# Kernel tuning notes

Hardware: AMD Instinct MI355X
Metric: run time of the kernel (lower is better)

## Reference

```python
import jax, jax.numpy as jnp
import numpy as np

EMBED_DIM = 1024
NUM_HEADS = 16
HEAD_DIM = EMBED_DIM // NUM_HEADS


def setup_inputs() -> dict:
    key = jax.random.key(0)
    ks = jax.random.split(key, 9)
    B, S, E, hd = 2, 2048, EMBED_DIM, HEAD_DIM
    s_e = 1.0 / np.sqrt(E)
    return {
        "x": jax.random.normal(ks[0], (B, S, E), dtype=jnp.float32),
        "wq": jax.random.uniform(ks[1], (E, E), jnp.float32, -s_e, s_e),
        "bq": jax.random.uniform(ks[2], (E,), jnp.float32, -s_e, s_e),
        "wk": jax.random.uniform(ks[3], (E, hd), jnp.float32, -s_e, s_e),
        "bk": jax.random.uniform(ks[4], (hd,), jnp.float32, -s_e, s_e),
        "wv": jax.random.uniform(ks[5], (E, hd), jnp.float32, -s_e, s_e),
        "bv": jax.random.uniform(ks[6], (hd,), jnp.float32, -s_e, s_e),
        "wo": jax.random.uniform(ks[7], (E, E), jnp.float32, -s_e, s_e),
        "bo": jax.random.uniform(ks[8], (E,), jnp.float32, -s_e, s_e),
    }


def reference(x, wq, bq, wk, bk, wv, bv, wo, bo):
    B, S, E = x.shape
    H, hd = NUM_HEADS, HEAD_DIM
    # projections
    q = (x @ wq + bq).reshape(B, S, H, hd)          # [B,S,H,hd]
    k = x @ wk + bk                                  # [B,S,hd] shared across heads
    v = x @ wv + bv                                  # [B,S,hd]
    scale = 1.0 / np.sqrt(hd).astype(np.float32)
    # scores: [B,H,S_q,S_k]
    scores = jnp.einsum('bqhd,bkd->bhqk', q, k) * scale
    attn = jax.nn.softmax(scores, axis=-1)
    out = jnp.einsum('bhqk,bkd->bqhd', attn, v).reshape(B, S, E)
    return out @ wo + bo
```

## Files before the change

kernel.cpp:

```cpp
#include <hip/hip_runtime.h>
#include <stdint.h>

#define SLEN 2048
#define EDIM 1024
#define NH 16
#define HD 64
#define QLD 1152

typedef unsigned short u16;
typedef short bf8 __attribute__((ext_vector_type(8)));
typedef float f4 __attribute__((ext_vector_type(4)));
typedef bf8 bf8_a __attribute__((may_alias));
typedef uint2 uint2_a __attribute__((may_alias));
typedef uint4 uint4_a __attribute__((may_alias));

__device__ __forceinline__ float bf2f(u16 u) {
  union { unsigned u; float f; } c; c.u = ((unsigned)u) << 16; return c.f;
}
__device__ __forceinline__ u16 f2bf(float x) {
  union { __bf16 h; u16 u; } c; c.h = (__bf16)x; return c.u;
}
__device__ __forceinline__ unsigned pk2bf(float a, float b) {
  union { __bf16 h[2]; unsigned u; } c;
  c.h[0] = (__bf16)a; c.h[1] = (__bf16)b;
  return c.u;
}
__device__ __forceinline__ void async_cp16(u16* lds, const u16* g) {
  __builtin_amdgcn_global_load_lds((__attribute__((address_space(1))) void*)g,
                                   (__attribute__((address_space(3))) void*)lds,
                                   16, 0, 0);
}

__global__ void probe_dtype(const unsigned* __restrict__ x, int* __restrict__ flag) {
  __shared__ int red[256];
  const int t = threadIdx.x;
  int cnt = 0;
  for (int i = t; i < 1024; i += 256) {
    unsigned e = (x[i] >> 7) & 0xFFu;
    cnt += (e >= 0x70u && e <= 0x8Fu) ? 1 : 0;
  }
  red[t] = cnt;
  __syncthreads();
  for (int s = 128; s > 0; s >>= 1) {
    if (t < s) red[t] += red[t + s];
    __syncthreads();
  }
  if (t == 0) *flag = (red[0] >= 512) ? 1 : 0;
}

__global__ void convert_x(const void* __restrict__ src, u16* __restrict__ dst,
                          const int* __restrict__ flag) {
  const int i = (blockIdx.x * 256 + threadIdx.x) * 8;
  if (*flag) {
    *(uint4_a*)&dst[i] = *(const uint4_a*)((const u16*)src + i);
  } else {
    const float* s = (const float*)src;
    u16 tmp[8];
#pragma unroll
    for (int j = 0; j < 8; ++j) tmp[j] = f2bf(s[i + j]);
    *(uint4_a*)&dst[i] = *(const uint4_a*)tmp;
  }
}

__device__ __forceinline__ void tcvt_tile(const void* src, int srcLd,
                                          u16* dst, int dstLd, int r0, int c0,
                                          bool isbf) {
  __shared__ u16 tile[64][65];
  const int t = threadIdx.x;
#pragma unroll
  for (int i = 0; i < 16; ++i) {
    int e = i * 256 + t, rr = e >> 6, cc = e & 63;
    size_t idx = (size_t)(r0 + rr) * srcLd + c0 + cc;
    tile[rr][cc] = isbf ? ((const u16*)src)[idx] : f2bf(((const float*)src)[idx]);
  }
  __syncthreads();
#pragma unroll
  for (int i = 0; i < 16; ++i) {
    int e = i * 256 + t, j = e >> 6, ii = e & 63;
    dst[(size_t)(c0 + j) * dstLd + r0 + ii] = tile[ii][j];
  }
}

__global__ void tcvt_qo(const void* wq, u16* wT, const void* wo, u16* woT,
                        const int* __restrict__ flag) {
  const bool isbf = (*flag != 0);
  const int yy = blockIdx.y;
  if (yy < 16) tcvt_tile(wq, 1024, wT, 1024, blockIdx.x * 64, yy * 64, isbf);
  else         tcvt_tile(wo, 1024, woT, 1024, blockIdx.x * 64, (yy - 16) * 64, isbf);
}
__global__ void tcvt_kv(const void* wk, const void* wv, u16* wT,
                        const int* __restrict__ flag) {
  const bool isbf = (*flag != 0);
  if (blockIdx.y == 0)
    tcvt_tile(wk, 64, wT + (size_t)1024 * 1024, 1024, blockIdx.x * 64, 0, isbf);
  else
    tcvt_tile(wv, 64, wT + (size_t)1088 * 1024, 1024, blockIdx.x * 64, 0, isbf);
}

__global__ void tpose_v(const u16* __restrict__ qkvb, u16* __restrict__ vTb) {
  __shared__ u16 tile[64][65];
  const int b = blockIdx.y, r0 = blockIdx.x * 64;
  const u16* src = qkvb + (size_t)b * SLEN * QLD + 1088;
  u16* dst = vTb + (size_t)b * 64 * SLEN;
  const int t = threadIdx.x;
#pragma unroll
  for (int i = 0; i < 16; ++i) {
    int e = i * 256 + t, rr = e >> 6, cc = e & 63;
    tile[rr][cc] = src[(size_t)(r0 + rr) * QLD + cc];
  }
  __syncthreads();
#pragma unroll
  for (int i = 0; i < 16; ++i) {
    int e = i * 256 + t, j = e >> 6, ii = e & 63;
    dst[(size_t)j * SLEN + r0 + ii] = tile[ii][j];
  }
}

__global__ void prep_bias(const void* bq, const void* bk, const void* bv,
                          const void* bo, float* biasQKV, float* biasOut,
                          const int* __restrict__ flag) {
  const bool isbf = (*flag != 0);
  int i = blockIdx.x * 256 + threadIdx.x;
  auto rd = [&](const void* p, int idx) -> float {
    return isbf ? bf2f(((const u16*)p)[idx]) : ((const float*)p)[idx];
  };
  if (i < 1024) biasQKV[i] = rd(bq, i);
  else if (i < 1088) biasQKV[i] = rd(bk, i - 1024);
  else if (i < 1152) biasQKV[i] = rd(bv, i - 1088);
  int j = i - 1152;
  if (j >= 0 && j < 1024) biasOut[j] = rd(bo, j);
}

__global__ __launch_bounds__(256) void gemm_bt_bias(
    const u16* __restrict__ A, const u16* __restrict__ Bt,
    const float* __restrict__ bias, void* __restrict__ C, int K, int ldc,
    int ofp32) {
  __shared__ __align__(16) u16 As[128 * 64];
  __shared__ __align__(16) u16 Bs[128 * 64];
  const int tn0 = blockIdx.x * 128, tm0 = blockIdx.y * 128;
  const int tid = threadIdx.x, wave = tid >> 6, lane = tid & 63;
  const int quad = lane >> 4, l16 = lane & 15;
  const int wm = wave & 1, wn = wave >> 1;

  f4 acc[4][4];
#pragma unroll
  for (int i = 0; i < 4; ++i)
#pragma unroll
    for (int j = 0; j < 4; ++j) acc[i][j] = f4{0.f, 0.f, 0.f, 0.f};

  int slot[4]; size_t aoff[4], boff[4];
#pragma unroll
  for (int i = 0; i < 4; ++i) {
    int s = i * 256 + tid, m = s >> 3, kc = s & 7, c = (kc - m) & 7;
    slot[i] = s;
    aoff[i] = (size_t)(tm0 + m) * K + c * 8;
    boff[i] = (size_t)(tn0 + m) * K + c * 8;
  }
  int ard[4][2], brd[4][2];
#pragma unroll
  for (int mi = 0; mi < 4; ++mi) {
    int m = wm * 64 + mi * 16 + l16;
#pragma unroll
    for (int kk = 0; kk < 2; ++kk)
      ard[mi][kk] = (m * 8 + (((kk * 4 + quad) + m) & 7)) * 8;
  }
#pragma unroll
  for (int ni = 0; ni < 4; ++ni) {
    int n = wn * 64 + ni * 16 + l16;
#pragma unroll
    for (int kk = 0; kk < 2; ++kk)
      brd[ni][kk] = (n * 8 + (((kk * 4 + quad) + n) & 7)) * 8;
  }

  const int kIt = K >> 6;
  for (int it = 0; it < kIt; ++it) {
    __syncthreads();
    const size_t kb = (size_t)it * 64;
#pragma unroll
    for (int i = 0; i < 4; ++i) {
      async_cp16(&As[slot[i] * 8], A + aoff[i] + kb);
      async_cp16(&Bs[slot[i] * 8], Bt + boff[i] + kb);
    }
    __syncthreads();
#pragma unroll
    for (int kk = 0; kk < 2; ++kk) {
      bf8 af[4], bfr[4];
#pragma unroll
      for (int mi = 0; mi < 4; ++mi) af[mi] = *(const bf8_a*)&As[ard[mi][kk]];
#pragma unroll
      for (int ni = 0; ni < 4; ++ni) bfr[ni] = *(const bf8_a*)&Bs[brd[ni][kk]];
#pragma unroll
      for (int mi = 0; mi < 4; ++mi)
#pragma unroll
        for (int ni = 0; ni < 4; ++ni)
          acc[mi][ni] = __builtin_amdgcn_mfma_f32_16x16x32_bf16(
              af[mi], bfr[ni], acc[mi][ni], 0, 0, 0);
    }
  }

  float bv[4];
#pragma unroll
  for (int ni = 0; ni < 4; ++ni) bv[ni] = bias[tn0 + wn * 64 + ni * 16 + l16];
#pragma unroll
  for (int mi = 0; mi < 4; ++mi) {
    int row0 = tm0 + wm * 64 + mi * 16 + quad * 4;
#pragma unroll
    for (int ni = 0; ni < 4; ++ni) {
      int col = tn0 + wn * 64 + ni * 16 + l16;
#pragma unroll
      for (int r = 0; r < 4; ++r) {
        float v = acc[mi][ni][r] + bv[ni];
        if (ofp32) ((float*)C)[(size_t)(row0 + r) * ldc + col] = v;
        else       ((u16*)C)[(size_t)(row0 + r) * ldc + col] = f2bf(v);
      }
    }
  }
}

__global__ __launch_bounds__(256, 2) void attn_kernel(
    const u16* __restrict__ qkv, const u16* __restrict__ vT,
    u16* __restrict__ aout) {
  __shared__ __align__(16) u16 Kf[8192];
  __shared__ __align__(16) u16 Vf[8192];
  __shared__ __align__(16) u16 Ps[16384];
  const int qt = blockIdx.x, bh = blockIdx.y, b = bh >> 4, h = bh & 15;
  const int tid = threadIdx.x, wave = tid >> 6, lane = tid & 63;
  const int quad = lane >> 4, l16 = lane & 15;

#pragma unroll
  for (int i = 0; i < 4; ++i) {
    int d = i * 256 + tid;
    int kk = d >> 9, g = (d >> 6) & 7, qd = (d >> 4) & 3, r16 = d & 15;
    async_cp16(&Kf[d * 8],
               qkv + (size_t)(b * SLEN + qt * 128 + g * 16 + r16) * QLD +
                   h * HD + (kk * 4 + qd) * 8);
  }
  __syncthreads();
  bf8 bq[2][2];
#pragma unroll
  for (int nt = 0; nt < 2; ++nt)
#pragma unroll
    for (int kk = 0; kk < 2; ++kk)
      bq[nt][kk] = *(const bf8_a*)&Kf[((kk * 8 + wave * 2 + nt) * 64 + lane) * 8];

  f4 acc_o[2][4];
#pragma unroll
  for (int i = 0; i < 2; ++i)
#pragma unroll
    for (int j = 0; j < 4; ++j) acc_o[i][j] = f4{0.f, 0.f, 0.f, 0.f};
  f4 lr4[2] = {f4{0.f, 0.f, 0.f, 0.f}, f4{0.f, 0.f, 0.f, 0.f}};
  const float C1 = 0.125f * 1.44269504089f;

  for (int kt = 0; kt < 16; ++kt) {
    __syncthreads();
#pragma unroll
    for (int i = 0; i < 4; ++i) {
      int d = i * 256 + tid;
      int kk = d >> 9, k8 = (d >> 6) & 7, qd = (d >> 4) & 3, r16 = d & 15;
      async_cp16(&Kf[d * 8],
                 qkv + (size_t)(b * SLEN + kt * 128 + k8 * 16 + r16) * QLD +
                     EDIM + (kk * 4 + qd) * 8);
    }
#pragma unroll
    for (int i = 0; i < 4; ++i) {
      int d = i * 256 + tid;
      int k4 = d >> 8, ni = (d >> 6) & 3, qd = (d >> 4) & 3, r16 = d & 15;
      async_cp16(&Vf[d * 8],
                 vT + (size_t)(b * 64 + ni * 16 + r16) * SLEN + kt * 128 +
                     (k4 * 4 + qd) * 8);
    }
    __syncthreads();

    f4 st[8][2];
#pragma unroll
    for (int k8 = 0; k8 < 8; ++k8)
#pragma unroll
      for (int nt = 0; nt < 2; ++nt) st[k8][nt] = f4{0.f, 0.f, 0.f, 0.f};
#pragma unroll
    for (int kk = 0; kk < 2; ++kk)
#pragma unroll
      for (int k8 = 0; k8 < 8; ++k8) {
        bf8 ak = *(const bf8_a*)&Kf[((kk * 8 + k8) * 64 + lane) * 8];
#pragma unroll
        for (int nt = 0; nt < 2; ++nt)
          st[k8][nt] = __builtin_amdgcn_mfma_f32_16x16x32_bf16(ak, bq[nt][kk], st[k8][nt], 0, 0, 0);
      }

#pragma unroll
    for (int nt = 0; nt < 2; ++nt)
#pragma unroll
      for (int k8 = 0; k8 < 8; ++k8) {
        f4 pe;
        pe[0] = __builtin_amdgcn_exp2f(st[k8][nt][0] * C1);
        pe[1] = __builtin_amdgcn_exp2f(st[k8][nt][1] * C1);
        pe[2] = __builtin_amdgcn_exp2f(st[k8][nt][2] * C1);
        pe[3] = __builtin_amdgcn_exp2f(st[k8][nt][3] * C1);
        lr4[nt] += pe;
        uint2 pk;
        pk.x = pk2bf(pe[0], pe[1]);
        pk.y = pk2bf(pe[2], pe[3]);
        int c = nt * 256 + (k8 >> 1) * 64 + (((k8 << 1) + (quad >> 1)) & 3) * 16 + l16;
        *(uint2_a*)&Ps[(wave * 512 + c) * 8 + (quad & 1) * 4] = pk;
      }
    __syncthreads();

#pragma unroll
    for (int k4 = 0; k4 < 4; ++k4) {
      bf8 ap[2];
#pragma unroll
      for (int mt = 0; mt < 2; ++mt)
        ap[mt] = *(const bf8_a*)&Ps[(wave * 512 + mt * 256 + k4 * 64 + quad * 16 + l16) * 8];
#pragma unroll
      for (int ni = 0; ni < 4; ++ni) {
        bf8 bv = *(const bf8_a*)&Vf[((k4 * 4 + ni) * 64 + lane) * 8];
#pragma unroll
        for (int mt = 0; mt < 2; ++mt)
          acc_o[mt][ni] = __builtin_amdgcn_mfma_f32_16x16x32_bf16(ap[mt], bv, acc_o[mt][ni], 0, 0, 0);
      }
    }
  }

  float ls[2];
#pragma unroll
  for (int nt = 0; nt < 2; ++nt) {
    float s = (lr4[nt][0] + lr4[nt][1]) + (lr4[nt][2] + lr4[nt][3]);
    s += __shfl_xor(s, 16, 64);
    s += __shfl_xor(s, 32, 64);
    ls[nt] = s;
  }
#pragma unroll
  for (int mt = 0; mt < 2; ++mt)
#pragma unroll
    for (int r = 0; r < 4; ++r) {
      float li = __shfl(ls[mt], quad * 4 + r, 64);
      float inv = 1.f / li;
      size_t row = (size_t)(b * SLEN + qt * 128 + wave * 32 + mt * 16 + quad * 4 + r);
#pragma unroll
      for (int ni = 0; ni < 4; ++ni)
        aout[row * EDIM + h * HD + ni * 16 + l16] = f2bf(acc_o[mt][ni][r] * inv);
    }
}

extern "C" void kernel_launch(void* const* d_in, const int* in_sizes, int n_in,
                              void* d_out, int out_size, void* d_ws, size_t ws_size,
                              hipStream_t stream) {
  const void* x  = d_in[0];
  const void* wq = d_in[1];
  const void* bq = d_in[2];
  const void* wk = d_in[3];
  const void* bk = d_in[4];
  const void* wv = d_in[5];
  const void* bv = d_in[6];
  const void* wo = d_in[7];
  const void* bo = d_in[8];

  char* ws = (char*)d_ws;
  size_t off = 0;
  auto carve = [&](size_t bytes) {
    void* p = ws + off;
    off = (off + bytes + 255) & ~(size_t)255;
    return p;
  };
  int* dflag   = (int*)carve(256);
  u16* xbf     = (u16*)carve((size_t)4096 * EDIM * 2);
  u16* wT      = (u16*)carve((size_t)1152 * 1024 * 2);
  u16* woT     = (u16*)carve((size_t)1024 * 1024 * 2);
  float* bQKV  = (float*)carve(1152 * 4);
  float* bOut  = (float*)carve(1024 * 4);
  u16* qkvb    = (u16*)carve((size_t)4096 * QLD * 2);
  u16* vTb     = (u16*)carve((size_t)2 * 64 * SLEN * 2);
  u16* aob     = (u16*)carve((size_t)4096 * EDIM * 2);

  probe_dtype<<<dim3(1), 256, 0, stream>>>((const unsigned*)x, dflag);
  convert_x<<<dim3(2048), 256, 0, stream>>>(x, xbf, dflag);
  tcvt_qo<<<dim3(16, 32), 256, 0, stream>>>(wq, wT, wo, woT, dflag);
  tcvt_kv<<<dim3(16, 2), 256, 0, stream>>>(wk, wv, wT, dflag);
  prep_bias<<<dim3(9), 256, 0, stream>>>(bq, bk, bv, bo, bQKV, bOut, dflag);

  gemm_bt_bias<<<dim3(9, 32), 256, 0, stream>>>(xbf, wT, bQKV, qkvb, 1024, QLD, 0);

  tpose_v<<<dim3(32, 2), 256, 0, stream>>>(qkvb, vTb);

  attn_kernel<<<dim3(16, 32), 256, 0, stream>>>(qkvb, vTb, aob);

  gemm_bt_bias<<<dim3(8, 32), 256, 0, stream>>>(aob, woT, bOut, d_out, 1024, 1024, 1);
}
```

Baseline: 210.5 us.

## Drop dtype probe, merge prep kernels, fuse V transpose, shrink GEMM tiles, per-chunk softmax

Removes the runtime dtype probe and assumes fp32 inputs, then merges the weight transpose and bias prep into one launch. The V transpose now happens in the QKV GEMM epilogue instead of a separate kernel. GEMM M-tiles shrink to 64 rows to launch more blocks. The attention kernel computes scores and P chunk by chunk per wave, which cuts P shared memory and raises the occupancy hint to 4 blocks per CU. Fewer launches and better occupancy come at the cost of less B-tile reuse in the GEMMs and of dropping bf16 input support.

```diff
diff --git a/kernel.cpp b/kernel.cpp
--- a/kernel.cpp
+++ b/kernel.cpp
@@ -14,9 +14,6 @@
 typedef uint2 uint2_a __attribute__((may_alias));
 typedef uint4 uint4_a __attribute__((may_alias));
 
-__device__ __forceinline__ float bf2f(u16 u) {
-  union { unsigned u; float f; } c; c.u = ((unsigned)u) << 16; return c.f;
-}
 __device__ __forceinline__ u16 f2bf(float x) {
   union { __bf16 h; u16 u; } c; c.h = (__bf16)x; return c.u;
 }
@@ -31,47 +28,22 @@
                                    16, 0, 0);
 }
 
-__global__ void probe_dtype(const unsigned* __restrict__ x, int* __restrict__ flag) {
-  __shared__ int red[256];
-  const int t = threadIdx.x;
-  int cnt = 0;
-  for (int i = t; i < 1024; i += 256) {
-    unsigned e = (x[i] >> 7) & 0xFFu;
-    cnt += (e >= 0x70u && e <= 0x8Fu) ? 1 : 0;
-  }
-  red[t] = cnt;
-  __syncthreads();
-  for (int s = 128; s > 0; s >>= 1) {
-    if (t < s) red[t] += red[t + s];
-    __syncthreads();
-  }
-  if (t == 0) *flag = (red[0] >= 512) ? 1 : 0;
-}
-
-__global__ void convert_x(const void* __restrict__ src, u16* __restrict__ dst,
-                          const int* __restrict__ flag) {
+__global__ void convert_x(const float* __restrict__ src, u16* __restrict__ dst) {
   const int i = (blockIdx.x * 256 + threadIdx.x) * 8;
-  if (*flag) {
-    *(uint4_a*)&dst[i] = *(const uint4_a*)((const u16*)src + i);
-  } else {
-    const float* s = (const float*)src;
-    u16 tmp[8];
-#pragma unroll
-    for (int j = 0; j < 8; ++j) tmp[j] = f2bf(s[i + j]);
-    *(uint4_a*)&dst[i] = *(const uint4_a*)tmp;
-  }
-}
-
-__device__ __forceinline__ void tcvt_tile(const void* src, int srcLd,
-                                          u16* dst, int dstLd, int r0, int c0,
-                                          bool isbf) {
+  u16 tmp[8];
+#pragma unroll
+  for (int j = 0; j < 8; ++j) tmp[j] = f2bf(src[i + j]);
+  *(uint4_a*)&dst[i] = *(const uint4_a*)tmp;
+}
+
+__device__ __forceinline__ void tcvt_tile(const float* src, int srcLd,
+                                          u16* dst, int dstLd, int r0, int c0) {
   __shared__ u16 tile[64][65];
   const int t = threadIdx.x;
 #pragma unroll
   for (int i = 0; i < 16; ++i) {
     int e = i * 256 + t, rr = e >> 6, cc = e & 63;
-    size_t idx = (size_t)(r0 + rr) * srcLd + c0 + cc;
-    tile[rr][cc] = isbf ? ((const u16*)src)[idx] : f2bf(((const float*)src)[idx]);
+    tile[rr][cc] = f2bf(src[(size_t)(r0 + rr) * srcLd + c0 + cc]);
   }
   __syncthreads();
 #pragma unroll
@@ -81,85 +53,57 @@
   }
 }
 
-__global__ void tcvt_qo(const void* wq, u16* wT, const void* wo, u16* woT,
-                        const int* __restrict__ flag) {
-  const bool isbf = (*flag != 0);
+__global__ void prep_w(const float* wq, const float* wk, const float* wv,
+                       const float* wo, const float* bq, const float* bk,
+                       const float* bv, const float* bo,
+                       u16* wT, u16* woT, float* bQKV, float* bOut) {
   const int yy = blockIdx.y;
-  if (yy < 16) tcvt_tile(wq, 1024, wT, 1024, blockIdx.x * 64, yy * 64, isbf);
-  else         tcvt_tile(wo, 1024, woT, 1024, blockIdx.x * 64, (yy - 16) * 64, isbf);
-}
-__global__ void tcvt_kv(const void* wk, const void* wv, u16* wT,
-                        const int* __restrict__ flag) {
-  const bool isbf = (*flag != 0);
-  if (blockIdx.y == 0)
-    tcvt_tile(wk, 64, wT + (size_t)1024 * 1024, 1024, blockIdx.x * 64, 0, isbf);
-  else
-    tcvt_tile(wv, 64, wT + (size_t)1088 * 1024, 1024, blockIdx.x * 64, 0, isbf);
-}
-
-__global__ void tpose_v(const u16* __restrict__ qkvb, u16* __restrict__ vTb) {
-  __shared__ u16 tile[64][65];
-  const int b = blockIdx.y, r0 = blockIdx.x * 64;
-  const u16* src = qkvb + (size_t)b * SLEN * QLD + 1088;
-  u16* dst = vTb + (size_t)b * 64 * SLEN;
-  const int t = threadIdx.x;
-#pragma unroll
-  for (int i = 0; i < 16; ++i) {
-    int e = i * 256 + t, rr = e >> 6, cc = e & 63;
-    tile[rr][cc] = src[(size_t)(r0 + rr) * QLD + cc];
-  }
-  __syncthreads();
-#pragma unroll
-  for (int i = 0; i < 16; ++i) {
-    int e = i * 256 + t, j = e >> 6, ii = e & 63;
-    dst[(size_t)j * SLEN + r0 + ii] = tile[ii][j];
-  }
-}
-
-__global__ void prep_bias(const void* bq, const void* bk, const void* bv,
-                          const void* bo, float* biasQKV, float* biasOut,
-                          const int* __restrict__ flag) {
-  const bool isbf = (*flag != 0);
-  int i = blockIdx.x * 256 + threadIdx.x;
-  auto rd = [&](const void* p, int idx) -> float {
-    return isbf ? bf2f(((const u16*)p)[idx]) : ((const float*)p)[idx];
-  };
-  if (i < 1024) biasQKV[i] = rd(bq, i);
-  else if (i < 1088) biasQKV[i] = rd(bk, i - 1024);
-  else if (i < 1152) biasQKV[i] = rd(bv, i - 1088);
-  int j = i - 1152;
-  if (j >= 0 && j < 1024) biasOut[j] = rd(bo, j);
+  if (yy < 16) tcvt_tile(wq, 1024, wT, 1024, blockIdx.x * 64, yy * 64);
+  else if (yy < 32) tcvt_tile(wo, 1024, woT, 1024, blockIdx.x * 64, (yy - 16) * 64);
+  else if (yy == 32) tcvt_tile(wk, 64, wT + (size_t)1024 * 1024, 1024, blockIdx.x * 64, 0);
+  else if (yy == 33) tcvt_tile(wv, 64, wT + (size_t)1088 * 1024, 1024, blockIdx.x * 64, 0);
+  else {
+    int i = blockIdx.x * 256 + threadIdx.x;
+    if (i < 1024) bQKV[i] = bq[i];
+    else if (i < 1088) bQKV[i] = bk[i - 1024];
+    else if (i < 1152) bQKV[i] = bv[i - 1088];
+    int j = i - 1152;
+    if (j >= 0 && j < 1024) bOut[j] = bo[j];
+  }
 }
 
 __global__ __launch_bounds__(256) void gemm_bt_bias(
     const u16* __restrict__ A, const u16* __restrict__ Bt,
     const float* __restrict__ bias, void* __restrict__ C, int K, int ldc,
-    int ofp32) {
-  __shared__ __align__(16) u16 As[128 * 64];
+    int ofp32, u16* __restrict__ vtb) {
+  __shared__ __align__(16) u16 As[64 * 64];
   __shared__ __align__(16) u16 Bs[128 * 64];
-  const int tn0 = blockIdx.x * 128, tm0 = blockIdx.y * 128;
+  const int tn0 = blockIdx.x * 128, tm0 = blockIdx.y * 64;
   const int tid = threadIdx.x, wave = tid >> 6, lane = tid & 63;
   const int quad = lane >> 4, l16 = lane & 15;
   const int wm = wave & 1, wn = wave >> 1;
 
-  f4 acc[4][4];
-#pragma unroll
-  for (int i = 0; i < 4; ++i)
+  f4 acc[2][4];
+#pragma unroll
+  for (int i = 0; i < 2; ++i)
 #pragma unroll
     for (int j = 0; j < 4; ++j) acc[i][j] = f4{0.f, 0.f, 0.f, 0.f};
 
-  int slot[4]; size_t aoff[4], boff[4];
+  int aslot[2], bslot[4]; size_t aoff[2], boff[4];
+#pragma unroll
+  for (int i = 0; i < 2; ++i) {
+    int s = i * 256 + tid, m = s >> 3, kc = s & 7, c = (kc - m) & 7;
+    aslot[i] = s; aoff[i] = (size_t)(tm0 + m) * K + c * 8;
+  }
 #pragma unroll
   for (int i = 0; i < 4; ++i) {
-    int s = i * 256 + tid, m = s >> 3, kc = s & 7, c = (kc - m) & 7;
-    slot[i] = s;
-    aoff[i] = (size_t)(tm0 + m) * K + c * 8;
-    boff[i] = (size_t)(tn0 + m) * K + c * 8;
-  }
-  int ard[4][2], brd[4][2];
-#pragma unroll
-  for (int mi = 0; mi < 4; ++mi) {
-    int m = wm * 64 + mi * 16 + l16;
+    int s = i * 256 + tid, n = s >> 3, kc = s & 7, c = (kc - n) & 7;
+    bslot[i] = s; boff[i] = (size_t)(tn0 + n) * K + c * 8;
+  }
+  int ard[2][2], brd[4][2];
+#pragma unroll
+  for (int mi = 0; mi < 2; ++mi) {
+    int m = wm * 32 + mi * 16 + l16;
 #pragma unroll
     for (int kk = 0; kk < 2; ++kk)
       ard[mi][kk] = (m * 8 + (((kk * 4 + quad) + m) & 7)) * 8;
@@ -177,20 +121,19 @@
     __syncthreads();
     const size_t kb = (size_t)it * 64;
 #pragma unroll
-    for (int i = 0; i < 4; ++i) {
-      async_cp16(&As[slot[i] * 8], A + aoff[i] + kb);
-      async_cp16(&Bs[slot[i] * 8], Bt + boff[i] + kb);
-    }
+    for (int i = 0; i < 2; ++i) async_cp16(&As[aslot[i] * 8], A + aoff[i] + kb);
+#pragma unroll
+    for (int i = 0; i < 4; ++i) async_cp16(&Bs[bslot[i] * 8], Bt + boff[i] + kb);
     __syncthreads();
 #pragma unroll
     for (int kk = 0; kk < 2; ++kk) {
-      bf8 af[4], bfr[4];
-#pragma unroll
-      for (int mi = 0; mi < 4; ++mi) af[mi] = *(const bf8_a*)&As[ard[mi][kk]];
+      bf8 af[2], bfr[4];
+#pragma unroll
+      for (int mi = 0; mi < 2; ++mi) af[mi] = *(const bf8_a*)&As[ard[mi][kk]];
 #pragma unroll
       for (int ni = 0; ni < 4; ++ni) bfr[ni] = *(const bf8_a*)&Bs[brd[ni][kk]];
 #pragma unroll
-      for (int mi = 0; mi < 4; ++mi)
+      for (int mi = 0; mi < 2; ++mi)
 #pragma unroll
         for (int ni = 0; ni < 4; ++ni)
           acc[mi][ni] = __builtin_amdgcn_mfma_f32_16x16x32_bf16(
@@ -202,27 +145,40 @@
 #pragma unroll
   for (int ni = 0; ni < 4; ++ni) bv[ni] = bias[tn0 + wn * 64 + ni * 16 + l16];
 #pragma unroll
-  for (int mi = 0; mi < 4; ++mi) {
-    int row0 = tm0 + wm * 64 + mi * 16 + quad * 4;
+  for (int mi = 0; mi < 2; ++mi) {
+    int row0 = tm0 + wm * 32 + mi * 16 + quad * 4;
 #pragma unroll
     for (int ni = 0; ni < 4; ++ni) {
       int col = tn0 + wn * 64 + ni * 16 + l16;
-#pragma unroll
-      for (int r = 0; r < 4; ++r) {
-        float v = acc[mi][ni][r] + bv[ni];
-        if (ofp32) ((float*)C)[(size_t)(row0 + r) * ldc + col] = v;
-        else       ((u16*)C)[(size_t)(row0 + r) * ldc + col] = f2bf(v);
+      float vv[4];
+#pragma unroll
+      for (int r = 0; r < 4; ++r) vv[r] = acc[mi][ni][r] + bv[ni];
+      if (ofp32) {
+#pragma unroll
+        for (int r = 0; r < 4; ++r)
+          ((float*)C)[(size_t)(row0 + r) * ldc + col] = vv[r];
+      } else {
+#pragma unroll
+        for (int r = 0; r < 4; ++r)
+          ((u16*)C)[(size_t)(row0 + r) * ldc + col] = f2bf(vv[r]);
       }
-    }
-  }
-}
-
-__global__ __launch_bounds__(256, 2) void attn_kernel(
+      if (vtb != nullptr && col >= 1088) {
+        int d = col - 1088, bb = row0 >> 11, s0 = row0 & 2047;
+        uint2 pk;
+        pk.x = pk2bf(vv[0], vv[1]);
+        pk.y = pk2bf(vv[2], vv[3]);
+        *(uint2_a*)&vtb[(size_t)(bb * 64 + d) * SLEN + s0] = pk;
+      }
+    }
+  }
+}
+
+__global__ __launch_bounds__(256, 4) void attn_kernel(
     const u16* __restrict__ qkv, const u16* __restrict__ vT,
     u16* __restrict__ aout) {
   __shared__ __align__(16) u16 Kf[8192];
   __shared__ __align__(16) u16 Vf[8192];
-  __shared__ __align__(16) u16 Ps[16384];
+  __shared__ __align__(16) u16 Ps[4096];
   const int qt = blockIdx.x, bh = blockIdx.y, b = bh >> 4, h = bh & 15;
   const int tid = threadIdx.x, wave = tid >> 6, lane = tid & 63;
   const int quad = lane >> 4, l16 = lane & 15;
@@ -250,6 +206,7 @@
     for (int j = 0; j < 4; ++j) acc_o[i][j] = f4{0.f, 0.f, 0.f, 0.f};
   f4 lr4[2] = {f4{0.f, 0.f, 0.f, 0.f}, f4{0.f, 0.f, 0.f, 0.f}};
   const float C1 = 0.125f * 1.44269504089f;
+  const int psb = wave * 1024;
 
   for (int kt = 0; kt < 16; ++kt) {
     __syncthreads();
@@ -271,52 +228,53 @@
     }
     __syncthreads();
 
-    f4 st[8][2];
-#pragma unroll
-    for (int k8 = 0; k8 < 8; ++k8)
-#pragma unroll
-      for (int nt = 0; nt < 2; ++nt) st[k8][nt] = f4{0.f, 0.f, 0.f, 0.f};
-#pragma unroll
-    for (int kk = 0; kk < 2; ++kk)
-#pragma unroll
-      for (int k8 = 0; k8 < 8; ++k8) {
-        bf8 ak = *(const bf8_a*)&Kf[((kk * 8 + k8) * 64 + lane) * 8];
-#pragma unroll
-        for (int nt = 0; nt < 2; ++nt)
-          st[k8][nt] = __builtin_amdgcn_mfma_f32_16x16x32_bf16(ak, bq[nt][kk], st[k8][nt], 0, 0, 0);
-      }
-
-#pragma unroll
-    for (int nt = 0; nt < 2; ++nt)
-#pragma unroll
-      for (int k8 = 0; k8 < 8; ++k8) {
-        f4 pe;
-        pe[0] = __builtin_amdgcn_exp2f(st[k8][nt][0] * C1);
-        pe[1] = __builtin_amdgcn_exp2f(st[k8][nt][1] * C1);
-        pe[2] = __builtin_amdgcn_exp2f(st[k8][nt][2] * C1);
-        pe[3] = __builtin_amdgcn_exp2f(st[k8][nt][3] * C1);
-        lr4[nt] += pe;
-        uint2 pk;
-        pk.x = pk2bf(pe[0], pe[1]);
-        pk.y = pk2bf(pe[2], pe[3]);
-        int c = nt * 256 + (k8 >> 1) * 64 + (((k8 << 1) + (quad >> 1)) & 3) * 16 + l16;
-        *(uint2_a*)&Ps[(wave * 512 + c) * 8 + (quad & 1) * 4] = pk;
-      }
-    __syncthreads();
-
 #pragma unroll
     for (int k4 = 0; k4 < 4; ++k4) {
+      f4 st[2][2];
+#pragma unroll
+      for (int j = 0; j < 2; ++j)
+#pragma unroll
+        for (int nt = 0; nt < 2; ++nt) st[j][nt] = f4{0.f, 0.f, 0.f, 0.f};
+#pragma unroll
+      for (int kk = 0; kk < 2; ++kk)
+#pragma unroll
+        for (int j = 0; j < 2; ++j) {
+          bf8 ak = *(const bf8_a*)&Kf[((kk * 8 + k4 * 2 + j) * 64 + lane) * 8];
+#pragma unroll
+          for (int nt = 0; nt < 2; ++nt)
+            st[j][nt] = __builtin_amdgcn_mfma_f32_16x16x32_bf16(
+                ak, bq[nt][kk], st[j][nt], 0, 0, 0);
+        }
+#pragma unroll
+      for (int nt = 0; nt < 2; ++nt)
+#pragma unroll
+        for (int j = 0; j < 2; ++j) {
+          f4 pe;
+          pe[0] = __builtin_amdgcn_exp2f(st[j][nt][0] * C1);
+          pe[1] = __builtin_amdgcn_exp2f(st[j][nt][1] * C1);
+          pe[2] = __builtin_amdgcn_exp2f(st[j][nt][2] * C1);
+          pe[3] = __builtin_amdgcn_exp2f(st[j][nt][3] * C1);
+          lr4[nt] += pe;
+          uint2 pk;
+          pk.x = pk2bf(pe[0], pe[1]);
+          pk.y = pk2bf(pe[2], pe[3]);
+          int qd2 = j * 2 + (quad >> 1);
+          *(uint2_a*)&Ps[psb + ((nt * 4 + qd2) * 16 + l16) * 8 + (quad & 1) * 4] = pk;
+        }
+      asm volatile("" ::: "memory");
       bf8 ap[2];
 #pragma unroll
       for (int mt = 0; mt < 2; ++mt)
-        ap[mt] = *(const bf8_a*)&Ps[(wave * 512 + mt * 256 + k4 * 64 + quad * 16 + l16) * 8];
+        ap[mt] = *(const bf8_a*)&Ps[psb + ((mt * 4 + quad) * 16 + l16) * 8];
 #pragma unroll
       for (int ni = 0; ni < 4; ++ni) {
         bf8 bv = *(const bf8_a*)&Vf[((k4 * 4 + ni) * 64 + lane) * 8];
 #pragma unroll
         for (int mt = 0; mt < 2; ++mt)
-          acc_o[mt][ni] = __builtin_amdgcn_mfma_f32_16x16x32_bf16(ap[mt], bv, acc_o[mt][ni], 0, 0, 0);
+          acc_o[mt][ni] = __builtin_amdgcn_mfma_f32_16x16x32_bf16(
+              ap[mt], bv, acc_o[mt][ni], 0, 0, 0);
       }
+      asm volatile("" ::: "memory");
     }
   }
 
@@ -344,15 +302,15 @@
 extern "C" void kernel_launch(void* const* d_in, const int* in_sizes, int n_in,
                               void* d_out, int out_size, void* d_ws, size_t ws_size,
                               hipStream_t stream) {
-  const void* x  = d_in[0];
-  const void* wq = d_in[1];
-  const void* bq = d_in[2];
-  const void* wk = d_in[3];
-  const void* bk = d_in[4];
-  const void* wv = d_in[5];
-  const void* bv = d_in[6];
-  const void* wo = d_in[7];
-  const void* bo = d_in[8];
+  const float* x  = (const float*)d_in[0];
+  const float* wq = (const float*)d_in[1];
+  const float* bq = (const float*)d_in[2];
+  const float* wk = (const float*)d_in[3];
+  const float* bk = (const float*)d_in[4];
+  const float* wv = (const float*)d_in[5];
+  const float* bv = (const float*)d_in[6];
+  const float* wo = (const float*)d_in[7];
+  const float* bo = (const float*)d_in[8];
 
   char* ws = (char*)d_ws;
   size_t off = 0;
@@ -361,7 +319,6 @@
     off = (off + bytes + 255) & ~(size_t)255;
     return p;
   };
-  int* dflag   = (int*)carve(256);
   u16* xbf     = (u16*)carve((size_t)4096 * EDIM * 2);
   u16* wT      = (u16*)carve((size_t)1152 * 1024 * 2);
   u16* woT     = (u16*)carve((size_t)1024 * 1024 * 2);
@@ -371,17 +328,15 @@
   u16* vTb     = (u16*)carve((size_t)2 * 64 * SLEN * 2);
   u16* aob     = (u16*)carve((size_t)4096 * EDIM * 2);
 
-  probe_dtype<<<dim3(1), 256, 0, stream>>>((const unsigned*)x, dflag);
-  convert_x<<<dim3(2048), 256, 0, stream>>>(x, xbf, dflag);
-  tcvt_qo<<<dim3(16, 32), 256, 0, stream>>>(wq, wT, wo, woT, dflag);
-  tcvt_kv<<<dim3(16, 2), 256, 0, stream>>>(wk, wv, wT, dflag);
-  prep_bias<<<dim3(9), 256, 0, stream>>>(bq, bk, bv, bo, bQKV, bOut, dflag);
-
-  gemm_bt_bias<<<dim3(9, 32), 256, 0, stream>>>(xbf, wT, bQKV, qkvb, 1024, QLD, 0);
-
-  tpose_v<<<dim3(32, 2), 256, 0, stream>>>(qkvb, vTb);
+  convert_x<<<dim3(2048), 256, 0, stream>>>(x, xbf);
+  prep_w<<<dim3(16, 35), 256, 0, stream>>>(wq, wk, wv, wo, bq, bk, bv, bo,
+                                           wT, woT, bQKV, bOut);
+
+  gemm_bt_bias<<<dim3(9, 64), 256, 0, stream>>>(xbf, wT, bQKV, qkvb, 1024, QLD,
+                                                0, vTb);
 
   attn_kernel<<<dim3(16, 32), 256, 0, stream>>>(qkvb, vTb, aob);
 
-  gemm_bt_bias<<<dim3(8, 32), 256, 0, stream>>>(aob, woT, bOut, d_out, 1024, 1024, 1);
-}
+  gemm_bt_bias<<<dim3(8, 64), 256, 0, stream>>>(aob, woT, bOut, d_out, 1024,
+                                                1024, 1, nullptr);
+}
```

Result: faster. 183.7 us (-12.7%).
